# Optimization experiments

Measured on AMD Instinct MI355X. Metric: run time of the kernel, lower is better.

The kernel has to match this reference:

```python
import jax, jax.numpy as jnp
from jax import lax
import numpy as np

RADIUS = 0.1
NSAMPLE = 32
STRIDE = 4
NUM_DIR = 32
BN_EPS = 1e-5


def _fps(p, m):
    # furthest point sampling: p (B,N,3) -> (B,m) int32 indices, start at index 0
    B, N, _ = p.shape

    def step(carry, _):
        dists, last = carry
        lp = jnp.take_along_axis(p, jnp.broadcast_to(last[:, None, None], (B, 1, 3)), axis=1)
        d = jnp.sum((p - lp) ** 2, axis=-1)
        dists = jnp.minimum(dists, d)
        nxt = jnp.argmax(dists, axis=-1).astype(jnp.int32)
        return (dists, nxt), nxt

    last0 = jnp.zeros((B,), jnp.int32)
    d0 = jnp.full((B, N), 1e10, p.dtype)
    _, rest = lax.scan(step, (d0, last0), None, length=m - 1)
    return jnp.concatenate([last0[None, :], rest], axis=0).T  # (B, m)


def _ball_query(q, p, k, radius):
    # q (B,M,3) centers, p (B,N,3) support -> (B,M,k) indices of first k points in ball,
    # padded with the first found index (PointNet++ convention)
    N = p.shape[1]
    d2 = jnp.sum((q[:, :, None, :] - p[:, None, :, :]) ** 2, axis=-1)  # (B,M,N)
    cand = jnp.where(d2 < radius * radius, jnp.arange(N, dtype=jnp.int32), N)
    cand = jnp.sort(cand, axis=-1)[:, :, :k]
    first = cand[:, :, :1]
    return jnp.where(cand == N, first, cand)


def _bn(x, g, b, m, v):
    # BatchNorm1d eval mode on (B,C,N)
    return (x - m[:, None]) * (g[:, None] / jnp.sqrt(v[:, None] + BN_EPS)) + b[:, None]


def _normalize(x, axis):
    return x / jnp.maximum(jnp.linalg.norm(x, axis=axis, keepdims=True), 1e-12)


def setup_inputs() -> dict:
    key = jax.random.key(0)
    ks = jax.random.split(key, 16)
    B, N, Cin, Cout = 4, 8192, 128, 256
    half = Cout // 2
    s = 0.02
    return {
        "p": jax.random.uniform(ks[0], (B, N, 3), jnp.float32),
        "f": jax.random.normal(ks[1], (B, Cin, N), jnp.float32),
        "conv1_w": jax.random.normal(ks[2], (Cout, Cin), jnp.float32) * s,
        "conv1_b": jax.random.normal(ks[3], (Cout,), jnp.float32) * s,
        "skip_w": jax.random.normal(ks[4], (Cout, Cin), jnp.float32) * s,
        "skip_b": jax.random.normal(ks[5], (Cout,), jnp.float32) * s,
        "bn1_g": jnp.ones((Cout,), jnp.float32),
        "bn1_b": jnp.zeros((Cout,), jnp.float32),
        "bn1_m": jax.random.normal(ks[6], (Cout,), jnp.float32) * 0.1,
        "bn1_v": jax.random.uniform(ks[7], (Cout,), jnp.float32) + 0.5,
        "dir_vectors": jax.random.normal(ks[8], (NUM_DIR, 3), jnp.float32),
        "de_w1": jax.random.normal(ks[9], (half, NUM_DIR), jnp.float32) * s,
        "de_g": jnp.ones((half,), jnp.float32),
        "de_bb": jnp.zeros((half,), jnp.float32),
        "de_m": jax.random.normal(ks[10], (half,), jnp.float32) * 0.1,
        "de_v": jax.random.uniform(ks[11], (half,), jnp.float32) + 0.5,
        "de_w2": jax.random.normal(ks[12], (Cout, half), jnp.float32) * s,
        "de_b2": jax.random.normal(ks[13], (Cout,), jnp.float32) * s,
    }


def reference(p, f, conv1_w, conv1_b, skip_w, skip_b, bn1_g, bn1_b, bn1_m, bn1_v,
              dir_vectors, de_w1, de_g, de_bb, de_m, de_v, de_w2, de_b2):
    B, N, _ = p.shape
    Cout = conv1_w.shape[0]
    M, K = N // STRIDE, NSAMPLE

    # FPS sampling + centroid gather
    idx = _fps(p, M)  # (B,M)
    new_p = jnp.take_along_axis(p, jnp.broadcast_to(idx[:, :, None], (B, M, 3)), axis=1)

    # residual branch: gather input feats at centroids, 1x1 conv (bn_after=False)
    fi = jnp.take_along_axis(f, jnp.broadcast_to(idx[:, None, :], (B, f.shape[1], M)), axis=2)
    identity = jnp.einsum('oc,bcm->bom', skip_w, fi) + skip_b[:, None]

    # convs1: 1x1 conv on all N points
    f1 = jnp.einsum('oc,bcn->bon', conv1_w, f) + conv1_b[:, None]  # (B,Cout,N)

    # ball-query grouping
    qidx = _ball_query(new_p, p, K, RADIUS)  # (B,M,K)
    idxf = qidx.reshape(B, M * K)
    gp = jnp.take_along_axis(p, jnp.broadcast_to(idxf[:, :, None], (B, M * K, 3)), axis=1).reshape(B, M, K, 3)
    dp = jnp.transpose(gp - new_p[:, :, None, :], (0, 3, 1, 2))  # (B,3,M,K)
    fj = jnp.take_along_axis(f1, jnp.broadcast_to(idxf[:, None, :], (B, Cout, M * K)), axis=2).reshape(B, Cout, M, K)

    # directional encoding
    dpn = _normalize(dp, axis=1)
    vec = _normalize(dir_vectors, axis=1)  # (NUM_DIR,3)
    theta = jnp.einsum('md,bdnk->bmnk', vec, dpn)  # (B,NUM_DIR,M,K)
    tmax = theta.max(axis=-1)  # (B,NUM_DIR,M)
    h = jnp.einsum('om,bmn->bon', de_w1, tmax)
    h = jax.nn.gelu(_bn(h, de_g, de_bb, de_m, de_v), approximate=False)
    pe = jnp.einsum('oc,bcn->bon', de_w2, h) + de_b2[:, None]

    # neighbor max-pool + BN + residuals
    f_out = _bn(fj.max(axis=-1), bn1_g, bn1_b, bn1_m, bn1_v) + pe + identity
    return new_p, f_out
```

## Files before the change

kernel.cpp:

```cpp
#include <hip/hip_runtime.h>

#define BATCH 4
#define NPTS 8192
#define MPTS 2048
#define CIN 128
#define CO 256
#define KS 32
#define ND 32
#define HALF 128

typedef unsigned int u32;
typedef unsigned long long u64;

#define DPPC_QUAD_XOR1 0xB1
#define DPPC_QUAD_XOR2 0x4E
#define DPPC_ROW_MIRROR 0x140
#define DPPC_ROW_HALF_MIRROR 0x141
#define DPPC_ROW_BCAST15 0x142
#define DPPC_ROW_BCAST31 0x143

template<int CTRL>
__device__ __forceinline__ float dpp_max(float v) {
    int o = __builtin_amdgcn_update_dpp(__float_as_int(-1e30f), __float_as_int(v),
                                        CTRL, 0xF, 0xF, false);
    return fmaxf(v, __int_as_float(o));
}
__device__ __forceinline__ float wave_max_f32(float v) {
    v = dpp_max<DPPC_QUAD_XOR1>(v);
    v = dpp_max<DPPC_QUAD_XOR2>(v);
    v = dpp_max<DPPC_ROW_HALF_MIRROR>(v);
    v = dpp_max<DPPC_ROW_MIRROR>(v);
    v = dpp_max<DPPC_ROW_BCAST15>(v);
    v = dpp_max<DPPC_ROW_BCAST31>(v);
    return __int_as_float(__builtin_amdgcn_readlane(__float_as_int(v), 63));
}

__global__ __launch_bounds__(512) void k_fps_f1(
    const float* __restrict__ p, const float* __restrict__ f,
    const float* __restrict__ conv1_w, const float* __restrict__ conv1_b,
    float* __restrict__ out_newp, int* __restrict__ idx,
    float* __restrict__ f1t) {
    if (blockIdx.x < 4) {
        __shared__ u64 wkey[2][8];
        int b = blockIdx.x, t = threadIdx.x;
        int lane = t & 63, wid = t >> 6;
        int j0 = t * 16;
        const float* pb = p + (size_t)b * NPTS * 3;
        const float* pt = pb + t * 48;
        float dist[16];
#pragma unroll
        for (int i = 0; i < 16; ++i) dist[i] = 1e10f;
        float lx = pb[0], ly = pb[1], lz = pb[2];
        if (t == 0) {
            out_newp[(size_t)b * MPTS * 3 + 0] = lx;
            out_newp[(size_t)b * MPTS * 3 + 1] = ly;
            out_newp[(size_t)b * MPTS * 3 + 2] = lz;
            idx[b * MPTS] = 0;
        }
        for (int s = 1; s < MPTS; ++s) {
            int par = s & 1;
            float bv = -1e30f; int bi = 0;
#pragma unroll
            for (int c = 0; c < 4; ++c) {
                float4 q0 = *(const float4*)(pt + c * 12 + 0);
                float4 q1 = *(const float4*)(pt + c * 12 + 4);
                float4 q2 = *(const float4*)(pt + c * 12 + 8);
                float cx[4] = { q0.x, q0.w, q1.z, q2.y };
                float cy[4] = { q0.y, q1.x, q1.w, q2.z };
                float cz[4] = { q0.z, q1.y, q2.x, q2.w };
#pragma unroll
                for (int i = 0; i < 4; ++i) {
                    float dx = __fsub_rn(cx[i], lx);
                    float dy = __fsub_rn(cy[i], ly);
                    float dz = __fsub_rn(cz[i], lz);
                    float d  = __fadd_rn(__fadd_rn(__fmul_rn(dx, dx), __fmul_rn(dy, dy)),
                                         __fmul_rn(dz, dz));
                    int li = c * 4 + i;
                    float nd = fminf(dist[li], d);
                    dist[li] = nd;
                    bool gt = nd > bv;
                    bi = gt ? li : bi;
                    bv = fmaxf(bv, nd);
                }
            }
            float gmw = wave_max_f32(bv);
            u64 mask = __ballot(bv == gmw);
            int first = __ffsll((long long)mask) - 1;
            if (lane == first) {
                wkey[par][wid] = ((u64)__float_as_uint(gmw) << 32)
                               | (u64)(u32)(NPTS - 1 - (j0 + bi));
            }
            __syncthreads();
            u64 bestk = wkey[par][0];
#pragma unroll
            for (int ww = 1; ww < 8; ++ww) {
                u64 kk = wkey[par][ww];
                if (kk > bestk) bestk = kk;
            }
            int w0 = (NPTS - 1 - (int)(bestk & 0xFFFFFFFFull)) & (NPTS - 1);
            lx = pb[w0 * 3 + 0]; ly = pb[w0 * 3 + 1]; lz = pb[w0 * 3 + 2];
            if (t == 0) {
                idx[b * MPTS + s] = w0;
                out_newp[((size_t)b * MPTS + s) * 3 + 0] = lx;
                out_newp[((size_t)b * MPTS + s) * 3 + 1] = ly;
                out_newp[((size_t)b * MPTS + s) * 3 + 2] = lz;
            }
        }
    } else if (f1t != nullptr) {
        __shared__ __align__(16) float fT[CIN * 32];
        int blk = blockIdx.x - 4;
        int b = blk >> 8;
        int n0 = (blk & 255) << 5;
        int t = threadIdx.x;
        const float* fb = f + (size_t)b * CIN * NPTS;
        for (int e = t; e < CIN * 32; e += 512) {
            int k = e >> 5, j = e & 31;
            fT[e] = fb[(size_t)k * NPTS + n0 + j];
        }
        __syncthreads();
        int c = t & 255, jh = (t >> 8) << 4;
        float bias = conv1_b[c];
        float acc[16];
#pragma unroll
        for (int j = 0; j < 16; ++j) acc[j] = bias;
        const float4* wrow4 = (const float4*)(conv1_w + (size_t)c * CIN);
        const float4* fT4 = (const float4*)fT;
        for (int k4 = 0; k4 < 32; ++k4) {
            float4 wv = wrow4[k4];
#pragma unroll
            for (int sub = 0; sub < 4; ++sub) {
                float w = sub == 0 ? wv.x : sub == 1 ? wv.y : sub == 2 ? wv.z : wv.w;
                int k = k4 * 4 + sub;
                int base = (k * 32 + jh) >> 2;
                float4 a0 = fT4[base+0], a1 = fT4[base+1], a2 = fT4[base+2], a3 = fT4[base+3];
                acc[0]  = fmaf(w, a0.x, acc[0]);  acc[1]  = fmaf(w, a0.y, acc[1]);
                acc[2]  = fmaf(w, a0.z, acc[2]);  acc[3]  = fmaf(w, a0.w, acc[3]);
                acc[4]  = fmaf(w, a1.x, acc[4]);  acc[5]  = fmaf(w, a1.y, acc[5]);
                acc[6]  = fmaf(w, a1.z, acc[6]);  acc[7]  = fmaf(w, a1.w, acc[7]);
                acc[8]  = fmaf(w, a2.x, acc[8]);  acc[9]  = fmaf(w, a2.y, acc[9]);
                acc[10] = fmaf(w, a2.z, acc[10]); acc[11] = fmaf(w, a2.w, acc[11]);
                acc[12] = fmaf(w, a3.x, acc[12]); acc[13] = fmaf(w, a3.y, acc[13]);
                acc[14] = fmaf(w, a3.z, acc[14]); acc[15] = fmaf(w, a3.w, acc[15]);
            }
        }
        float* dst = f1t + ((size_t)b * NPTS + n0 + jh) * CO + c;
#pragma unroll
        for (int j = 0; j < 16; ++j) dst[(size_t)j * CO] = acc[j];
    }
}

__global__ __launch_bounds__(256) void k_f1(const float* __restrict__ f,
                                            const float* __restrict__ conv1_w,
                                            const float* __restrict__ conv1_b,
                                            float* __restrict__ f1t, int b0) {
    __shared__ __align__(16) float fT[CIN * 16];
    int blk = blockIdx.x;
    int bl = blk >> 9;
    int b = b0 + bl;
    int n0 = (blk & 511) << 4;
    int t = threadIdx.x;
    const float* fb = f + (size_t)b * CIN * NPTS;
    for (int e = t; e < CIN * 16; e += 256) {
        int k = e >> 4, j = e & 15;
        fT[e] = fb[(size_t)k * NPTS + n0 + j];
    }
    __syncthreads();
    int c = t;
    float bias = conv1_b[c];
    float acc[16];
#pragma unroll
    for (int j = 0; j < 16; ++j) acc[j] = bias;
    const float4* wrow4 = (const float4*)(conv1_w + (size_t)c * CIN);
    const float4* fT4 = (const float4*)fT;
    for (int k4 = 0; k4 < 32; ++k4) {
        float4 wv = wrow4[k4];
#pragma unroll
        for (int sub = 0; sub < 4; ++sub) {
            float w = sub == 0 ? wv.x : sub == 1 ? wv.y : sub == 2 ? wv.z : wv.w;
            int k = k4 * 4 + sub;
            float4 a0 = fT4[k*4+0], a1 = fT4[k*4+1], a2 = fT4[k*4+2], a3 = fT4[k*4+3];
            acc[0]  = fmaf(w, a0.x, acc[0]);  acc[1]  = fmaf(w, a0.y, acc[1]);
            acc[2]  = fmaf(w, a0.z, acc[2]);  acc[3]  = fmaf(w, a0.w, acc[3]);
            acc[4]  = fmaf(w, a1.x, acc[4]);  acc[5]  = fmaf(w, a1.y, acc[5]);
            acc[6]  = fmaf(w, a1.z, acc[6]);  acc[7]  = fmaf(w, a1.w, acc[7]);
            acc[8]  = fmaf(w, a2.x, acc[8]);  acc[9]  = fmaf(w, a2.y, acc[9]);
            acc[10] = fmaf(w, a2.z, acc[10]); acc[11] = fmaf(w, a2.w, acc[11]);
            acc[12] = fmaf(w, a3.x, acc[12]); acc[13] = fmaf(w, a3.y, acc[13]);
            acc[14] = fmaf(w, a3.z, acc[14]); acc[15] = fmaf(w, a3.w, acc[15]);
        }
    }
    float* dst = f1t + ((size_t)bl * NPTS + n0) * CO + c;
#pragma unroll
    for (int j = 0; j < 16; ++j) dst[(size_t)j * CO] = acc[j];
}

__global__ __launch_bounds__(256) void k_feat(
    const float* __restrict__ p, const float* __restrict__ f,
    const float* __restrict__ f1t,
    const float* __restrict__ skip_w,  const float* __restrict__ skip_b,
    const float* __restrict__ bn1_g, const float* __restrict__ bn1_b,
    const float* __restrict__ bn1_m, const float* __restrict__ bn1_v,
    const float* __restrict__ dirv,  const float* __restrict__ de_w1,
    const float* __restrict__ de_g,  const float* __restrict__ de_bb,
    const float* __restrict__ de_m,  const float* __restrict__ de_v,
    const float* __restrict__ de_w2, const float* __restrict__ de_b2,
    const int* __restrict__ idx,     float* __restrict__ out_f, int b0) {
    __shared__ float sdx[KS], sdy[KS], sdz[KS];
    __shared__ float ltm[ND], lfi[CIN], lh[HALF];
    __shared__ int swidx[4][KS];
    __shared__ int scnt[4];
    __shared__ int nb[KS], nbp[KS];

    int q = b0 * MPTS + blockIdx.x;
    int b = q >> 11;
    int bl = b - b0;
    int m = q & (MPTS - 1);
    int t = threadIdx.x, lane = t & 63, w = t >> 6;
    const float* pb = p + (size_t)b * NPTS * 3;
    int i0 = idx[q] & (NPTS - 1);
    float qx = pb[i0 * 3 + 0], qy = pb[i0 * 3 + 1], qz = pb[i0 * 3 + 2];
    const float R2 = 0.1f * 0.1f;

    int cnt = 0;
    int seg = w * 2048;
    for (int base = 0; base < 2048; base += 64) {
        int j = seg + base + lane;
        float dx = __fsub_rn(pb[j * 3 + 0], qx);
        float dy = __fsub_rn(pb[j * 3 + 1], qy);
        float dz = __fsub_rn(pb[j * 3 + 2], qz);
        float d2 = __fadd_rn(__fadd_rn(__fmul_rn(dx, dx), __fmul_rn(dy, dy)),
                             __fmul_rn(dz, dz));
        bool hit = d2 < R2;
        u64 mask = __ballot(hit);
        if (hit) {
            int pos = cnt + __popcll(mask & ((1ull << lane) - 1ull));
            if (pos < KS) swidx[w][pos] = j;
        }
        cnt += __popcll(mask);
        if (cnt >= KS) break;
    }
    if (lane == 0) scnt[w] = cnt < KS ? cnt : KS;
    __syncthreads();
    int c0s = scnt[0], c1s = scnt[1], c2s = scnt[2], c3s = scnt[3];
    int st1 = c0s, st2 = c0s + c1s, st3 = c0s + c1s + c2s;
    int total = c0s + c1s + c2s + c3s; if (total > KS) total = KS;
    if (total < 1) total = 1;
    if (t < 128) {
        int ww = t >> 5, l = t & 31;
        int stw = (ww == 0) ? 0 : (ww == 1) ? st1 : (ww == 2) ? st2 : st3;
        int cw  = (ww == 0) ? c0s : (ww == 1) ? c1s : (ww == 2) ? c2s : c3s;
        int gp = stw + l;
        if (l < cw && gp < KS) nb[gp] = swidx[ww][l];
    }
    __syncthreads();
    if (t < KS) {
        int jk = nb[t < total ? t : 0] & (NPTS - 1);
        nbp[t] = jk;
        float dx = pb[jk * 3 + 0] - qx;
        float dy = pb[jk * 3 + 1] - qy;
        float dz = pb[jk * 3 + 2] - qz;
        float nr = fmaxf(sqrtf(dx * dx + dy * dy + dz * dz), 1e-12f);
        sdx[t] = dx / nr; sdy[t] = dy / nr; sdz[t] = dz / nr;
    }
    if (t >= 128) {
        lfi[t - 128] = f[((size_t)b * CIN + (t - 128)) * NPTS + i0];
    }
    __syncthreads();
    if (t < ND) {
        float ax = dirv[t * 3], ay = dirv[t * 3 + 1], az = dirv[t * 3 + 2];
        float n = fmaxf(sqrtf(ax * ax + ay * ay + az * az), 1e-12f);
        float vx = ax / n, vy = ay / n, vz = az / n;
        float tm = -1e30f;
#pragma unroll
        for (int k = 0; k < KS; ++k)
            tm = fmaxf(tm, vx * sdx[k] + vy * sdy[k] + vz * sdz[k]);
        ltm[t] = tm;
    }
    __syncthreads();

    int c = t;
    const float* f1b = f1t + (size_t)bl * NPTS * CO + c;
    float mx = -1e30f;
#pragma unroll 8
    for (int k = 0; k < KS; ++k) {
        mx = fmaxf(mx, f1b[(size_t)nbp[k] * CO]);
    }
    float sc1 = bn1_g[c] / sqrtf(bn1_v[c] + 1e-5f);
    float o1 = (mx - bn1_m[c]) * sc1 + bn1_b[c];

    float idv = skip_b[c];
    {
        const float4* sr = (const float4*)(skip_w + (size_t)c * CIN);
#pragma unroll 8
        for (int r = 0; r < 32; ++r) {
            float4 v = sr[r];
            idv = fmaf(v.x, lfi[r*4+0], fmaf(v.y, lfi[r*4+1],
                  fmaf(v.z, lfi[r*4+2], fmaf(v.w, lfi[r*4+3], idv))));
        }
    }
    {
        int hc = c & (HALF - 1);
        const float4* d1 = (const float4*)(de_w1 + (size_t)hc * ND);
        float a = 0.0f;
#pragma unroll
        for (int r = 0; r < 8; ++r) {
            float4 v = d1[r];
            a = fmaf(v.x, ltm[r*4+0], fmaf(v.y, ltm[r*4+1],
                fmaf(v.z, ltm[r*4+2], fmaf(v.w, ltm[r*4+3], a))));
        }
        float dsc = de_g[hc] / sqrtf(de_v[hc] + 1e-5f);
        float xb = (a - de_m[hc]) * dsc + de_bb[hc];
        float hv = 0.5f * xb * (1.0f + erff(xb * 0.70710678118654752440f));
        if (c < HALF) lh[c] = hv;
    }
    __syncthreads();
    float pe = de_b2[c];
    {
        const float4* d2p = (const float4*)(de_w2 + (size_t)c * HALF);
#pragma unroll 8
        for (int r = 0; r < 32; ++r) {
            float4 v = d2p[r];
            pe = fmaf(v.x, lh[r*4+0], fmaf(v.y, lh[r*4+1],
                 fmaf(v.z, lh[r*4+2], fmaf(v.w, lh[r*4+3], pe))));
        }
    }
    out_f[((size_t)b * CO + c) * MPTS + m] = o1 + pe + idv;
}

__global__ __launch_bounds__(256) void k_featz_fused(
    const float* __restrict__ p, const float* __restrict__ f,
    const float* __restrict__ conv1_w, const float* __restrict__ conv1_b,
    const float* __restrict__ skip_w,  const float* __restrict__ skip_b,
    const float* __restrict__ bn1_g, const float* __restrict__ bn1_b,
    const float* __restrict__ bn1_m, const float* __restrict__ bn1_v,
    const float* __restrict__ dirv,  const float* __restrict__ de_w1,
    const float* __restrict__ de_g,  const float* __restrict__ de_bb,
    const float* __restrict__ de_m,  const float* __restrict__ de_v,
    const float* __restrict__ de_w2, const float* __restrict__ de_b2,
    const int* __restrict__ idx,     float* __restrict__ out_f) {
    __shared__ __align__(16) float fg[KS * CIN];
    __shared__ float sdx[KS], sdy[KS], sdz[KS];
    __shared__ float ltm[ND], lfi[CIN], lh[HALF];
    __shared__ int swidx[4][KS];
    __shared__ int scnt[4];
    __shared__ int nb[KS], nbp[KS];

    int q = blockIdx.x;
    int b = q >> 11;
    int m = q & (MPTS - 1);
    int t = threadIdx.x, lane = t & 63, w = t >> 6;
    const float* pb = p + (size_t)b * NPTS * 3;
    int i0 = idx[q] & (NPTS - 1);
    float qx = pb[i0 * 3 + 0], qy = pb[i0 * 3 + 1], qz = pb[i0 * 3 + 2];
    const float R2 = 0.1f * 0.1f;
    int cnt = 0;
    int seg = w * 2048;
    for (int base = 0; base < 2048; base += 64) {
        int j = seg + base + lane;
        float dx = __fsub_rn(pb[j * 3 + 0], qx);
        float dy = __fsub_rn(pb[j * 3 + 1], qy);
        float dz = __fsub_rn(pb[j * 3 + 2], qz);
        float d2 = __fadd_rn(__fadd_rn(__fmul_rn(dx, dx), __fmul_rn(dy, dy)),
                             __fmul_rn(dz, dz));
        bool hit = d2 < R2;
        u64 mask = __ballot(hit);
        if (hit) {
            int pos = cnt + __popcll(mask & ((1ull << lane) - 1ull));
            if (pos < KS) swidx[w][pos] = j;
        }
        cnt += __popcll(mask);
        if (cnt >= KS) break;
    }
    if (lane == 0) scnt[w] = cnt < KS ? cnt : KS;
    __syncthreads();
    int c0s = scnt[0], c1s = scnt[1], c2s = scnt[2], c3s = scnt[3];
    int st1 = c0s, st2 = c0s + c1s, st3 = c0s + c1s + c2s;
    int total = c0s + c1s + c2s + c3s; if (total > KS) total = KS;
    if (total < 1) total = 1;
    if (t < 128) {
        int ww = t >> 5, l = t & 31;
        int stw = (ww == 0) ? 0 : (ww == 1) ? st1 : (ww == 2) ? st2 : st3;
        int cw  = (ww == 0) ? c0s : (ww == 1) ? c1s : (ww == 2) ? c2s : c3s;
        int gp = stw + l;
        if (l < cw && gp < KS) nb[gp] = swidx[ww][l];
    }
    __syncthreads();
    if (t < KS) {
        int jk = nb[t < total ? t : 0] & (NPTS - 1);
        nbp[t] = jk;
        float dx = pb[jk * 3 + 0] - qx;
        float dy = pb[jk * 3 + 1] - qy;
        float dz = pb[jk * 3 + 2] - qz;
        float nr = fmaxf(sqrtf(dx * dx + dy * dy + dz * dz), 1e-12f);
        sdx[t] = dx / nr; sdy[t] = dy / nr; sdz[t] = dz / nr;
    }
    if (t >= 128) lfi[t - 128] = f[((size_t)b * CIN + (t - 128)) * NPTS + i0];
    __syncthreads();
    if (t < ND) {
        float ax = dirv[t * 3], ay = dirv[t * 3 + 1], az = dirv[t * 3 + 2];
        float n = fmaxf(sqrtf(ax * ax + ay * ay + az * az), 1e-12f);
        float vx = ax / n, vy = ay / n, vz = az / n;
        float tm = -1e30f;
#pragma unroll
        for (int k = 0; k < KS; ++k)
            tm = fmaxf(tm, vx * sdx[k] + vy * sdy[k] + vz * sdz[k]);
        ltm[t] = tm;
    }
    for (int e = t; e < KS * CIN; e += 256) {
        int k = e >> 7, i = e & 127;
        fg[k * CIN + i] = f[((size_t)b * CIN + i) * NPTS + nbp[k]];
    }
    __syncthreads();
    int c = t;
    float acc[KS];
#pragma unroll
    for (int k = 0; k < KS; ++k) acc[k] = 0.0f;
    const float4* w4 = (const float4*)(conv1_w + (size_t)c * CIN);
    const float4* fg4 = (const float4*)fg;
    for (int i4 = 0; i4 < 32; ++i4) {
        float4 wv = w4[i4];
#pragma unroll 8
        for (int k = 0; k < KS; ++k) {
            float4 g = fg4[k * 32 + i4];
            acc[k] = fmaf(wv.x, g.x, fmaf(wv.y, g.y,
                     fmaf(wv.z, g.z, fmaf(wv.w, g.w, acc[k]))));
        }
    }
    float bias = conv1_b[c];
    float mx = -1e30f;
#pragma unroll
    for (int k = 0; k < KS; ++k) mx = fmaxf(mx, acc[k] + bias);
    float sc1 = bn1_g[c] / sqrtf(bn1_v[c] + 1e-5f);
    float o1 = (mx - bn1_m[c]) * sc1 + bn1_b[c];
    float idv = skip_b[c];
    {
        const float4* sr = (const float4*)(skip_w + (size_t)c * CIN);
#pragma unroll 8
        for (int r = 0; r < 32; ++r) {
            float4 v = sr[r];
            idv = fmaf(v.x, lfi[r*4+0], fmaf(v.y, lfi[r*4+1],
                  fmaf(v.z, lfi[r*4+2], fmaf(v.w, lfi[r*4+3], idv))));
        }
    }
    {
        int hc = c & (HALF - 1);
        const float4* d1 = (const float4*)(de_w1 + (size_t)hc * ND);
        float a = 0.0f;
#pragma unroll
        for (int r = 0; r < 8; ++r) {
            float4 v = d1[r];
            a = fmaf(v.x, ltm[r*4+0], fmaf(v.y, ltm[r*4+1],
                fmaf(v.z, ltm[r*4+2], fmaf(v.w, ltm[r*4+3], a))));
        }
        float dsc = de_g[hc] / sqrtf(de_v[hc] + 1e-5f);
        float xb = (a - de_m[hc]) * dsc + de_bb[hc];
        float hv = 0.5f * xb * (1.0f + erff(xb * 0.70710678118654752440f));
        if (c < HALF) lh[c] = hv;
    }
    __syncthreads();
    float pe = de_b2[c];
    {
        const float4* d2p = (const float4*)(de_w2 + (size_t)c * HALF);
#pragma unroll 8
        for (int r = 0; r < 32; ++r) {
            float4 v = d2p[r];
            pe = fmaf(v.x, lh[r*4+0], fmaf(v.y, lh[r*4+1],
                 fmaf(v.z, lh[r*4+2], fmaf(v.w, lh[r*4+3], pe))));
        }
    }
    out_f[((size_t)b * CO + c) * MPTS + m] = o1 + pe + idv;
}

extern "C" void kernel_launch(void* const* d_in, const int* in_sizes, int n_in,
                              void* d_out, int out_size, void* d_ws, size_t ws_size,
                              hipStream_t stream) {
    const float* p       = (const float*)d_in[0];
    const float* f       = (const float*)d_in[1];
    const float* conv1_w = (const float*)d_in[2];
    const float* conv1_b = (const float*)d_in[3];
    const float* skip_w  = (const float*)d_in[4];
    const float* skip_b  = (const float*)d_in[5];
    const float* bn1_g   = (const float*)d_in[6];
    const float* bn1_b   = (const float*)d_in[7];
    const float* bn1_m   = (const float*)d_in[8];
    const float* bn1_v   = (const float*)d_in[9];
    const float* dirv    = (const float*)d_in[10];
    const float* de_w1   = (const float*)d_in[11];
    const float* de_g    = (const float*)d_in[12];
    const float* de_bb   = (const float*)d_in[13];
    const float* de_m    = (const float*)d_in[14];
    const float* de_v    = (const float*)d_in[15];
    const float* de_w2   = (const float*)d_in[16];
    const float* de_b2   = (const float*)d_in[17];

    float* out_newp = (float*)d_out;
    float* out_f    = (float*)d_out + (size_t)BATCH * MPTS * 3;
    int*   idx      = (int*)d_ws;
    float* f1t      = (float*)((char*)d_ws + 32768);

    size_t f1_one  = (size_t)NPTS * CO * 4;
    size_t need_full = 32768 + 4 * f1_one;
    size_t need_one  = 32768 + f1_one;
    int mode = (ws_size >= need_full) ? 2 : (ws_size >= need_one) ? 1 : 0;

    if (mode == 2) {
        k_fps_f1<<<dim3(4 + 1024), dim3(512), 0, stream>>>(
            p, f, conv1_w, conv1_b, out_newp, idx, f1t);
        k_feat<<<dim3(4 * MPTS), dim3(256), 0, stream>>>(
            p, f, f1t, skip_w, skip_b, bn1_g, bn1_b, bn1_m, bn1_v,
            dirv, de_w1, de_g, de_bb, de_m, de_v, de_w2, de_b2, idx, out_f, 0);
    } else if (mode == 1) {
        k_fps_f1<<<dim3(4), dim3(512), 0, stream>>>(
            p, f, conv1_w, conv1_b, out_newp, idx, nullptr);
        for (int b0 = 0; b0 < BATCH; ++b0) {
            k_f1  <<<dim3(512),  dim3(256), 0, stream>>>(f, conv1_w, conv1_b, f1t, b0);
            k_feat<<<dim3(MPTS), dim3(256), 0, stream>>>(
                p, f, f1t, skip_w, skip_b, bn1_g, bn1_b, bn1_m, bn1_v,
                dirv, de_w1, de_g, de_bb, de_m, de_v, de_w2, de_b2, idx, out_f, b0);
        }
    } else {
        k_fps_f1<<<dim3(4), dim3(512), 0, stream>>>(
            p, f, conv1_w, conv1_b, out_newp, idx, nullptr);
        k_featz_fused<<<dim3(BATCH * MPTS), dim3(256), 0, stream>>>(
            p, f, conv1_w, conv1_b, skip_w, skip_b, bn1_g, bn1_b, bn1_m, bn1_v,
            dirv, de_w1, de_g, de_bb, de_m, de_v, de_w2, de_b2, idx, out_f);
    }
}
```

Baseline: 2.814 ms.

## Widen FPS block to 1024 threads with xy cached in LDS and z in registers

The furthest-point-sampling block grows from 512 to 1024 threads, so each thread handles 8 points instead of 16. Point x/y coordinates are staged in dynamic shared memory (up to 8144 points fit in 64KB) and z stays in registers. This shortens the serial per-step distance loop and replaces the global reload of the selected point with an LDS read plus a z value published per wave. The per-wave argmax now uses a second u32 DPP reduction instead of ballot, and the fused f1 GEMM tile doubles to 64 points to match the larger block. The cost is a 16-way cross-wave reduction per step, heavier syncthreads with 16 waves, and a 64KB LDS footprint that limits occupancy for the GEMM blocks.

```diff
diff --git a/kernel.cpp b/kernel.cpp
--- a/kernel.cpp
+++ b/kernel.cpp
@@ -8,6 +8,7 @@
 #define KS 32
 #define ND 32
 #define HALF 128
+#define SXY_PTS 8144
 
 typedef unsigned int u32;
 typedef unsigned long long u64;
@@ -20,36 +21,60 @@
 #define DPPC_ROW_BCAST31 0x143
 
 template<int CTRL>
-__device__ __forceinline__ float dpp_max(float v) {
+__device__ __forceinline__ float dpp_max_f(float v) {
     int o = __builtin_amdgcn_update_dpp(__float_as_int(-1e30f), __float_as_int(v),
                                         CTRL, 0xF, 0xF, false);
     return fmaxf(v, __int_as_float(o));
 }
 __device__ __forceinline__ float wave_max_f32(float v) {
-    v = dpp_max<DPPC_QUAD_XOR1>(v);
-    v = dpp_max<DPPC_QUAD_XOR2>(v);
-    v = dpp_max<DPPC_ROW_HALF_MIRROR>(v);
-    v = dpp_max<DPPC_ROW_MIRROR>(v);
-    v = dpp_max<DPPC_ROW_BCAST15>(v);
-    v = dpp_max<DPPC_ROW_BCAST31>(v);
+    v = dpp_max_f<DPPC_QUAD_XOR1>(v);
+    v = dpp_max_f<DPPC_QUAD_XOR2>(v);
+    v = dpp_max_f<DPPC_ROW_HALF_MIRROR>(v);
+    v = dpp_max_f<DPPC_ROW_MIRROR>(v);
+    v = dpp_max_f<DPPC_ROW_BCAST15>(v);
+    v = dpp_max_f<DPPC_ROW_BCAST31>(v);
     return __int_as_float(__builtin_amdgcn_readlane(__float_as_int(v), 63));
 }
-
-__global__ __launch_bounds__(512) void k_fps_f1(
+template<int CTRL>
+__device__ __forceinline__ u32 dpp_max_u(u32 v) {
+    u32 o = (u32)__builtin_amdgcn_update_dpp(0, (int)v, CTRL, 0xF, 0xF, false);
+    return v > o ? v : o;
+}
+__device__ __forceinline__ u32 wave_max_u32(u32 v) {
+    v = dpp_max_u<DPPC_QUAD_XOR1>(v);
+    v = dpp_max_u<DPPC_QUAD_XOR2>(v);
+    v = dpp_max_u<DPPC_ROW_HALF_MIRROR>(v);
+    v = dpp_max_u<DPPC_ROW_MIRROR>(v);
+    v = dpp_max_u<DPPC_ROW_BCAST15>(v);
+    v = dpp_max_u<DPPC_ROW_BCAST31>(v);
+    return (u32)__builtin_amdgcn_readlane((int)v, 63);
+}
+
+__global__ __launch_bounds__(1024) void k_fps_f1(
     const float* __restrict__ p, const float* __restrict__ f,
     const float* __restrict__ conv1_w, const float* __restrict__ conv1_b,
     float* __restrict__ out_newp, int* __restrict__ idx,
     float* __restrict__ f1t) {
+    extern __shared__ __align__(16) char smem[];
     if (blockIdx.x < 4) {
-        __shared__ u64 wkey[2][8];
+        float2* sxy  = (float2*)smem;
+        u64*    wkey = (u64*)(smem + SXY_PTS * 8);
+        float*  wz   = (float*)(smem + SXY_PTS * 8 + 256);
         int b = blockIdx.x, t = threadIdx.x;
-        int lane = t & 63, wid = t >> 6;
-        int j0 = t * 16;
+        int lane = t & 63, w = t >> 6;
         const float* pb = p + (size_t)b * NPTS * 3;
-        const float* pt = pb + t * 48;
-        float dist[16];
-#pragma unroll
-        for (int i = 0; i < 16; ++i) dist[i] = 1e10f;
+        for (int j = t; j < SXY_PTS; j += 1024)
+            sxy[j] = make_float2(pb[j * 3 + 0], pb[j * 3 + 1]);
+        int jbase = w * 512 + lane * 2;
+        float z[8], dist[8];
+#pragma unroll
+        for (int c = 0; c < 4; ++c)
+#pragma unroll
+            for (int i = 0; i < 2; ++i) {
+                z[c * 2 + i] = pb[(jbase + c * 128 + i) * 3 + 2];
+                dist[c * 2 + i] = 1e10f;
+            }
+        __syncthreads();
         float lx = pb[0], ly = pb[1], lz = pb[2];
         if (t == 0) {
             out_newp[(size_t)b * MPTS * 3 + 0] = lx;
@@ -59,46 +84,57 @@
         }
         for (int s = 1; s < MPTS; ++s) {
             int par = s & 1;
-            float bv = -1e30f; int bi = 0;
+            float bv = -1e30f; int bg = 0, bl = 0;
 #pragma unroll
             for (int c = 0; c < 4; ++c) {
-                float4 q0 = *(const float4*)(pt + c * 12 + 0);
-                float4 q1 = *(const float4*)(pt + c * 12 + 4);
-                float4 q2 = *(const float4*)(pt + c * 12 + 8);
-                float cx[4] = { q0.x, q0.w, q1.z, q2.y };
-                float cy[4] = { q0.y, q1.x, q1.w, q2.z };
-                float cz[4] = { q0.z, q1.y, q2.x, q2.w };
-#pragma unroll
-                for (int i = 0; i < 4; ++i) {
-                    float dx = __fsub_rn(cx[i], lx);
-                    float dy = __fsub_rn(cy[i], ly);
-                    float dz = __fsub_rn(cz[i], lz);
+                int j = jbase + c * 128;
+                float x0, y0, x1, y1;
+                if (j < SXY_PTS) {
+                    float4 v = *(const float4*)&sxy[j];
+                    x0 = v.x; y0 = v.y; x1 = v.z; y1 = v.w;
+                } else {
+                    x0 = pb[j * 3 + 0]; y0 = pb[j * 3 + 1];
+                    x1 = pb[j * 3 + 3]; y1 = pb[j * 3 + 4];
+                }
+#pragma unroll
+                for (int i = 0; i < 2; ++i) {
+                    float px = i == 0 ? x0 : x1;
+                    float py = i == 0 ? y0 : y1;
+                    int li = c * 2 + i;
+                    float dx = __fsub_rn(px, lx);
+                    float dy = __fsub_rn(py, ly);
+                    float dz = __fsub_rn(z[li], lz);
                     float d  = __fadd_rn(__fadd_rn(__fmul_rn(dx, dx), __fmul_rn(dy, dy)),
                                          __fmul_rn(dz, dz));
-                    int li = c * 4 + i;
                     float nd = fminf(dist[li], d);
                     dist[li] = nd;
                     bool gt = nd > bv;
-                    bi = gt ? li : bi;
+                    bg = gt ? (j + i) : bg;
+                    bl = gt ? li : bl;
                     bv = fmaxf(bv, nd);
                 }
             }
             float gmw = wave_max_f32(bv);
-            u64 mask = __ballot(bv == gmw);
-            int first = __ffsll((long long)mask) - 1;
-            if (lane == first) {
-                wkey[par][wid] = ((u64)__float_as_uint(gmw) << 32)
-                               | (u64)(u32)(NPTS - 1 - (j0 + bi));
+            u32 mg = (bv == gmw) ? (u32)(NPTS - 1 - bg) : 0u;
+            u32 mmax = wave_max_u32(mg);
+            if (bv == gmw && (u32)(NPTS - 1 - bg) == mmax) {
+                float zz = z[0];
+#pragma unroll
+                for (int k = 1; k < 8; ++k) if (bl == k) zz = z[k];
+                wkey[par * 16 + w] = ((u64)__float_as_uint(gmw) << 32) | mmax;
+                wz[par * 16 + w] = zz;
             }
             __syncthreads();
-            u64 bestk = wkey[par][0];
-#pragma unroll
-            for (int ww = 1; ww < 8; ++ww) {
-                u64 kk = wkey[par][ww];
-                if (kk > bestk) bestk = kk;
+            u64 bestk = wkey[par * 16]; int bw = 0;
+#pragma unroll
+            for (int ww = 1; ww < 16; ++ww) {
+                u64 kk = wkey[par * 16 + ww];
+                if (kk > bestk) { bestk = kk; bw = ww; }
             }
             int w0 = (NPTS - 1 - (int)(bestk & 0xFFFFFFFFull)) & (NPTS - 1);
-            lx = pb[w0 * 3 + 0]; ly = pb[w0 * 3 + 1]; lz = pb[w0 * 3 + 2];
+            lz = wz[par * 16 + bw];
+            if (w0 < SXY_PTS) { float2 v = sxy[w0]; lx = v.x; ly = v.y; }
+            else { lx = pb[w0 * 3 + 0]; ly = pb[w0 * 3 + 1]; }
             if (t == 0) {
                 idx[b * MPTS + s] = w0;
                 out_newp[((size_t)b * MPTS + s) * 3 + 0] = lx;
@@ -107,14 +143,14 @@
             }
         }
     } else if (f1t != nullptr) {
-        __shared__ __align__(16) float fT[CIN * 32];
+        float* fT = (float*)smem;
         int blk = blockIdx.x - 4;
-        int b = blk >> 8;
-        int n0 = (blk & 255) << 5;
+        int b = blk >> 7;
+        int n0 = (blk & 127) << 6;
         int t = threadIdx.x;
         const float* fb = f + (size_t)b * CIN * NPTS;
-        for (int e = t; e < CIN * 32; e += 512) {
-            int k = e >> 5, j = e & 31;
+        for (int e = t; e < CIN * 64; e += 1024) {
+            int k = e >> 6, j = e & 63;
             fT[e] = fb[(size_t)k * NPTS + n0 + j];
         }
         __syncthreads();
@@ -129,18 +165,18 @@
             float4 wv = wrow4[k4];
 #pragma unroll
             for (int sub = 0; sub < 4; ++sub) {
-                float w = sub == 0 ? wv.x : sub == 1 ? wv.y : sub == 2 ? wv.z : wv.w;
+                float wgt = sub == 0 ? wv.x : sub == 1 ? wv.y : sub == 2 ? wv.z : wv.w;
                 int k = k4 * 4 + sub;
-                int base = (k * 32 + jh) >> 2;
+                int base = (k * 64 + jh) >> 2;
                 float4 a0 = fT4[base+0], a1 = fT4[base+1], a2 = fT4[base+2], a3 = fT4[base+3];
-                acc[0]  = fmaf(w, a0.x, acc[0]);  acc[1]  = fmaf(w, a0.y, acc[1]);
-                acc[2]  = fmaf(w, a0.z, acc[2]);  acc[3]  = fmaf(w, a0.w, acc[3]);
-                acc[4]  = fmaf(w, a1.x, acc[4]);  acc[5]  = fmaf(w, a1.y, acc[5]);
-                acc[6]  = fmaf(w, a1.z, acc[6]);  acc[7]  = fmaf(w, a1.w, acc[7]);
-                acc[8]  = fmaf(w, a2.x, acc[8]);  acc[9]  = fmaf(w, a2.y, acc[9]);
-                acc[10] = fmaf(w, a2.z, acc[10]); acc[11] = fmaf(w, a2.w, acc[11]);
-                acc[12] = fmaf(w, a3.x, acc[12]); acc[13] = fmaf(w, a3.y, acc[13]);
-                acc[14] = fmaf(w, a3.z, acc[14]); acc[15] = fmaf(w, a3.w, acc[15]);
+                acc[0]  = fmaf(wgt, a0.x, acc[0]);  acc[1]  = fmaf(wgt, a0.y, acc[1]);
+                acc[2]  = fmaf(wgt, a0.z, acc[2]);  acc[3]  = fmaf(wgt, a0.w, acc[3]);
+                acc[4]  = fmaf(wgt, a1.x, acc[4]);  acc[5]  = fmaf(wgt, a1.y, acc[5]);
+                acc[6]  = fmaf(wgt, a1.z, acc[6]);  acc[7]  = fmaf(wgt, a1.w, acc[7]);
+                acc[8]  = fmaf(wgt, a2.x, acc[8]);  acc[9]  = fmaf(wgt, a2.y, acc[9]);
+                acc[10] = fmaf(wgt, a2.z, acc[10]); acc[11] = fmaf(wgt, a2.w, acc[11]);
+                acc[12] = fmaf(wgt, a3.x, acc[12]); acc[13] = fmaf(wgt, a3.y, acc[13]);
+                acc[14] = fmaf(wgt, a3.z, acc[14]); acc[15] = fmaf(wgt, a3.w, acc[15]);
             }
         }
         float* dst = f1t + ((size_t)b * NPTS + n0 + jh) * CO + c;
@@ -176,17 +212,17 @@
         float4 wv = wrow4[k4];
 #pragma unroll
         for (int sub = 0; sub < 4; ++sub) {
-            float w = sub == 0 ? wv.x : sub == 1 ? wv.y : sub == 2 ? wv.z : wv.w;
+            float wgt = sub == 0 ? wv.x : sub == 1 ? wv.y : sub == 2 ? wv.z : wv.w;
             int k = k4 * 4 + sub;
             float4 a0 = fT4[k*4+0], a1 = fT4[k*4+1], a2 = fT4[k*4+2], a3 = fT4[k*4+3];
-            acc[0]  = fmaf(w, a0.x, acc[0]);  acc[1]  = fmaf(w, a0.y, acc[1]);
-            acc[2]  = fmaf(w, a0.z, acc[2]);  acc[3]  = fmaf(w, a0.w, acc[3]);
-            acc[4]  = fmaf(w, a1.x, acc[4]);  acc[5]  = fmaf(w, a1.y, acc[5]);
-            acc[6]  = fmaf(w, a1.z, acc[6]);  acc[7]  = fmaf(w, a1.w, acc[7]);
-            acc[8]  = fmaf(w, a2.x, acc[8]);  acc[9]  = fmaf(w, a2.y, acc[9]);
-            acc[10] = fmaf(w, a2.z, acc[10]); acc[11] = fmaf(w, a2.w, acc[11]);
-            acc[12] = fmaf(w, a3.x, acc[12]); acc[13] = fmaf(w, a3.y, acc[13]);
-            acc[14] = fmaf(w, a3.z, acc[14]); acc[15] = fmaf(w, a3.w, acc[15]);
+            acc[0]  = fmaf(wgt, a0.x, acc[0]);  acc[1]  = fmaf(wgt, a0.y, acc[1]);
+            acc[2]  = fmaf(wgt, a0.z, acc[2]);  acc[3]  = fmaf(wgt, a0.w, acc[3]);
+            acc[4]  = fmaf(wgt, a1.x, acc[4]);  acc[5]  = fmaf(wgt, a1.y, acc[5]);
+            acc[6]  = fmaf(wgt, a1.z, acc[6]);  acc[7]  = fmaf(wgt, a1.w, acc[7]);
+            acc[8]  = fmaf(wgt, a2.x, acc[8]);  acc[9]  = fmaf(wgt, a2.y, acc[9]);
+            acc[10] = fmaf(wgt, a2.z, acc[10]); acc[11] = fmaf(wgt, a2.w, acc[11]);
+            acc[12] = fmaf(wgt, a3.x, acc[12]); acc[13] = fmaf(wgt, a3.y, acc[13]);
+            acc[14] = fmaf(wgt, a3.z, acc[14]); acc[15] = fmaf(wgt, a3.w, acc[15]);
         }
     }
     float* dst = f1t + ((size_t)bl * NPTS + n0) * CO + c;
@@ -502,15 +538,16 @@
     size_t need_full = 32768 + 4 * f1_one;
     size_t need_one  = 32768 + f1_one;
     int mode = (ws_size >= need_full) ? 2 : (ws_size >= need_one) ? 1 : 0;
+    const size_t DYN = 65536;
 
     if (mode == 2) {
-        k_fps_f1<<<dim3(4 + 1024), dim3(512), 0, stream>>>(
+        k_fps_f1<<<dim3(4 + 512), dim3(1024), DYN, stream>>>(
             p, f, conv1_w, conv1_b, out_newp, idx, f1t);
         k_feat<<<dim3(4 * MPTS), dim3(256), 0, stream>>>(
             p, f, f1t, skip_w, skip_b, bn1_g, bn1_b, bn1_m, bn1_v,
             dirv, de_w1, de_g, de_bb, de_m, de_v, de_w2, de_b2, idx, out_f, 0);
     } else if (mode == 1) {
-        k_fps_f1<<<dim3(4), dim3(512), 0, stream>>>(
+        k_fps_f1<<<dim3(4), dim3(1024), DYN, stream>>>(
             p, f, conv1_w, conv1_b, out_newp, idx, nullptr);
         for (int b0 = 0; b0 < BATCH; ++b0) {
             k_f1  <<<dim3(512),  dim3(256), 0, stream>>>(f, conv1_w, conv1_b, f1t, b0);
@@ -519,7 +556,7 @@
                 dirv, de_w1, de_g, de_bb, de_m, de_v, de_w2, de_b2, idx, out_f, b0);
         }
     } else {
-        k_fps_f1<<<dim3(4), dim3(512), 0, stream>>>(
+        k_fps_f1<<<dim3(4), dim3(1024), DYN, stream>>>(
             p, f, conv1_w, conv1_b, out_newp, idx, nullptr);
         k_featz_fused<<<dim3(BATCH * MPTS), dim3(256), 0, stream>>>(
             p, f, conv1_w, conv1_b, skip_w, skip_b, bn1_g, bn1_b, bn1_m, bn1_v,
```

Result: slower. 3.803 ms (+35.1%).
